# Performance work log

Hardware: AMD Instinct MI355X
Metric: run time of the kernel (lower is better)

Reference implementation:

```python
import jax, jax.numpy as jnp
import numpy as np

NPML = 50
B, NZ, NX = 4, 1024, 1024


def diff_using_roll(x, dim, forward=True):
    # First-order staggered-grid difference via circular roll (PML absorbs the
    # wrap-around, matching seistorch's roll-based stencil).
    if forward:
        return jnp.roll(x, -1, axis=dim) - x
    return x - jnp.roll(x, 1, axis=dim)


def _pml_profile(nz, nx, npml):
    # Quadratic damping profile, zero in interior, rising in the PML pad.
    iz = np.arange(nz, dtype=np.float32)
    ix = np.arange(nx, dtype=np.float32)
    dz = np.maximum(npml - iz, iz - (nz - 1 - npml))
    dx = np.maximum(npml - ix, ix - (nx - 1 - npml))
    dz = np.clip(dz, 0.0, None) / npml
    dx = np.clip(dx, 0.0, None) / npml
    prof = np.maximum(dz[:, None], dx[None, :]) ** 2
    return jnp.asarray(100.0 * prof, dtype=jnp.float32)


def setup_inputs() -> dict:
    key = jax.random.key(0)
    ks = jax.random.split(key, 8)
    vp = 3000.0 + 500.0 * jax.random.uniform(ks[0], (NZ, NX), dtype=jnp.float32)
    vs = 1700.0 + 300.0 * jax.random.uniform(ks[1], (NZ, NX), dtype=jnp.float32)
    rho = 2100.0 + 300.0 * jax.random.uniform(ks[2], (NZ, NX), dtype=jnp.float32)
    vx = jax.random.normal(ks[3], (B, NZ, NX), dtype=jnp.float32)
    vz = jax.random.normal(ks[4], (B, NZ, NX), dtype=jnp.float32)
    txx = jax.random.normal(ks[5], (B, NZ, NX), dtype=jnp.float32)
    tzz = jax.random.normal(ks[6], (B, NZ, NX), dtype=jnp.float32)
    txz = jax.random.normal(ks[7], (B, NZ, NX), dtype=jnp.float32)
    dt = jnp.float32(0.001)
    h = jnp.float32(10.0)     # 10 m grid spacing
    d = _pml_profile(NZ, NX, NPML)
    return {"vp": vp, "vs": vs, "rho": rho, "vx": vx, "vz": vz,
            "txx": txx, "tzz": tzz, "txz": txz, "dt": dt, "h": h, "d": d}


def reference(vp, vs, rho, vx, vz, txx, tzz, txz, dt, h, d):
    # Elastic wave equation time step with PML damping (seistorch _time_step).
    lame_lambda = rho * (vp * vp - 2.0 * vs * vs)  # [NZ,NX], broadcasts over shots
    lame_mu = rho * vs * vs

    vx_x = diff_using_roll(vx, 2, False)
    vz_z = diff_using_roll(vz, 1, True)
    vx_z = diff_using_roll(vx, 1, True)
    vz_x = diff_using_roll(vz, 2, True)

    c = 0.5 * dt * d
    inv = 1.0 / (1.0 + c)
    dth = dt / h

    y_txx = inv * (dth * ((lame_lambda + 2.0 * lame_mu) * vx_x + lame_lambda * vz_z) + (1.0 - c) * txx)
    y_tzz = inv * (dth * ((lame_lambda + 2.0 * lame_mu) * vz_z + lame_lambda * vx_x) + (1.0 - c) * tzz)
    y_txz = inv * (dt * lame_mu / h * (vz_x + vx_z) + (1.0 - c) * txz)

    txx_x = diff_using_roll(y_txx, 2, True)
    txz_z = diff_using_roll(y_txz, 1, False)
    tzz_z = diff_using_roll(y_tzz, 1, False)
    txz_x = diff_using_roll(y_txz, 2, False)

    y_vx = inv * (dth / rho * (txx_x + txz_z) + (1.0 - c) * vx)
    y_vz = inv * (dth / rho * (txz_x + tzz_z) + (1.0 - c) * vz)

    return (y_vx, y_vz, y_txx, y_tzz, y_txz)
```

## Files before the change

kernel.cpp:

```cpp
#include <hip/hip_runtime.h>


constexpr int Bn = 4, NZ = 1024, NX = 1024;
constexpr int PLANE = NZ * NX;
constexpr int NPTS = Bn * PLANE;
constexpr int R = 8;
constexpr int NSTRIP = NZ / R;
constexpr int LOG_NSTRIP = 7;

__global__ __launch_bounds__(256, 2) void fused_wave_kernel(
    const float* __restrict__ vp, const float* __restrict__ vs,
    const float* __restrict__ rho, const float* __restrict__ vx,
    const float* __restrict__ vz, const float* __restrict__ txx,
    const float* __restrict__ tzz, const float* __restrict__ txz,
    const float* __restrict__ dtp, const float* __restrict__ hp,
    const float* __restrict__ dpml,
    float* __restrict__ y_vx, float* __restrict__ y_vz,
    float* __restrict__ y_txx, float* __restrict__ y_tzz,
    float* __restrict__ y_txz)
{
    __shared__ float s_txx[3][NX];
    __shared__ float s_tzz[3][NX];
    __shared__ float s_txz[3][NX];

    const int tid = threadIdx.x;
    const int x0 = tid * 4;
    const int xm1 = (x0 - 1) & (NX - 1);
    const int xp4 = (x0 + 4) & (NX - 1);
    const int strip = blockIdx.x & (NSTRIP - 1);
    const int b = blockIdx.x >> LOG_NSTRIP;
    const int z0 = strip * R;
    const size_t fb = (size_t)b * PLANE;

    const float dt = dtp[0], h = hp[0];
    const float dth = dt / h;

    const int r0 = (z0 - 1) & (NZ - 1);
    const int r1 = z0;
    const size_t rb0 = fb + (size_t)r0 * NX;
    const size_t rb1 = fb + (size_t)r1 * NX;
    const int m0 = r0 * NX;

    float4 cvx = *(const float4*)(vx + rb0 + x0);
    float4 cvz = *(const float4*)(vz + rb0 + x0);
    float4 nvx = *(const float4*)(vx + rb1 + x0);
    float4 nvz = *(const float4*)(vz + rb1 + x0);
    float  cvxm = vx[rb0 + xm1];
    float  cvzp = vz[rb0 + xp4];
    float4 ctxx = *(const float4*)(txx + rb0 + x0);
    float4 ctzz = *(const float4*)(tzz + rb0 + x0);
    float4 ctxz = *(const float4*)(txz + rb0 + x0);
    float4 cvp = *(const float4*)(vp + m0 + x0);
    float4 cvs = *(const float4*)(vs + m0 + x0);
    float4 crh = *(const float4*)(rho + m0 + x0);
    float4 cd  = *(const float4*)(dpml + m0 + x0);

#pragma unroll
    for (int k = 0; k <= R; ++k) {
        const int r = (z0 - 1 + k) & (NZ - 1);
        const size_t rowb = fb + (size_t)r * NX;

        float4 n2vx, n2vz, ntxx, ntzz, ntxz, nvp, nvs, nrh, nd;
        float  nvxm = 0.f, nvzp = 0.f;
        if (k < R) {
            const int rn  = (z0 + k) & (NZ - 1);
            const int rn2 = (z0 + k + 1) & (NZ - 1);
            const size_t rbn  = fb + (size_t)rn * NX;
            const size_t rbn2 = fb + (size_t)rn2 * NX;
            const int mn = rn * NX;
            n2vx = *(const float4*)(vx + rbn2 + x0);
            n2vz = *(const float4*)(vz + rbn2 + x0);
            nvxm = vx[rbn + xm1];
            nvzp = vz[rbn + xp4];
            ntxx = *(const float4*)(txx + rbn + x0);
            ntzz = *(const float4*)(tzz + rbn + x0);
            ntxz = *(const float4*)(txz + rbn + x0);
            nvp = *(const float4*)(vp + mn + x0);
            nvs = *(const float4*)(vs + mn + x0);
            nrh = *(const float4*)(rho + mn + x0);
            nd  = *(const float4*)(dpml + mn + x0);
        }

        float fvx[5]  = {cvxm, cvx.x, cvx.y, cvx.z, cvx.w};
        float fvz[5]  = {cvz.x, cvz.y, cvz.z, cvz.w, cvzp};
        float fvx1[4] = {nvx.x, nvx.y, nvx.z, nvx.w};
        float fvz1[4] = {nvz.x, nvz.y, nvz.z, nvz.w};
        float ftxxo[4] = {ctxx.x, ctxx.y, ctxx.z, ctxx.w};
        float ftzzo[4] = {ctzz.x, ctzz.y, ctzz.z, ctzz.w};
        float ftxzo[4] = {ctxz.x, ctxz.y, ctxz.z, ctxz.w};
        float fvp[4] = {cvp.x, cvp.y, cvp.z, cvp.w};
        float fvs[4] = {cvs.x, cvs.y, cvs.z, cvs.w};
        float frh[4] = {crh.x, crh.y, crh.z, crh.w};
        float fd[4]  = {cd.x, cd.y, cd.z, cd.w};

        float o_txx[4], o_tzz[4], o_txz[4], inv[4], omc[4];
#pragma unroll
        for (int i = 0; i < 4; ++i) {
            float lam = frh[i] * (fvp[i] * fvp[i] - 2.0f * fvs[i] * fvs[i]);
            float mu  = frh[i] * fvs[i] * fvs[i];
            float vx_x = fvx[i + 1] - fvx[i];
            float vz_z = fvz1[i] - fvz[i];
            float vx_z = fvx1[i] - fvx[i + 1];
            float vz_x = fvz[i + 1] - fvz[i];
            float c = 0.5f * dt * fd[i];
            inv[i] = 1.0f / (1.0f + c);
            omc[i] = 1.0f - c;
            float lp2m = lam + 2.0f * mu;
            o_txx[i] = inv[i] * (dth * (lp2m * vx_x + lam * vz_z) + omc[i] * ftxxo[i]);
            o_tzz[i] = inv[i] * (dth * (lp2m * vz_z + lam * vx_x) + omc[i] * ftzzo[i]);
            o_txz[i] = inv[i] * (dth * mu * (vz_x + vx_z) + omc[i] * ftxzo[i]);
        }

        const int slot = k % 3;
        const int pslot = (k + 2) % 3;
        *(float4*)&s_txx[slot][x0] = make_float4(o_txx[0], o_txx[1], o_txx[2], o_txx[3]);
        *(float4*)&s_tzz[slot][x0] = make_float4(o_tzz[0], o_tzz[1], o_tzz[2], o_tzz[3]);
        *(float4*)&s_txz[slot][x0] = make_float4(o_txz[0], o_txz[1], o_txz[2], o_txz[3]);
        if (k > 0) {
            *(float4*)(y_txx + rowb + x0) = make_float4(o_txx[0], o_txx[1], o_txx[2], o_txx[3]);
            *(float4*)(y_tzz + rowb + x0) = make_float4(o_tzz[0], o_tzz[1], o_tzz[2], o_tzz[3]);
            *(float4*)(y_txz + rowb + x0) = make_float4(o_txz[0], o_txz[1], o_txz[2], o_txz[3]);
        }

        asm volatile("s_waitcnt lgkmcnt(0)" ::: "memory");
        __builtin_amdgcn_s_barrier();

        if (k > 0) {
            float  txxp4v = s_txx[slot][xp4];
            float  txzm1v = s_txz[slot][xm1];
            float4 txzzm = *(const float4*)&s_txz[pslot][x0];
            float4 tzzzm = *(const float4*)&s_tzz[pslot][x0];

            float ftxx5[5] = {o_txx[0], o_txx[1], o_txx[2], o_txx[3], txxp4v};
            float ftxz5[5] = {txzm1v, o_txz[0], o_txz[1], o_txz[2], o_txz[3]};
            float ftxzzm[4] = {txzzm.x, txzzm.y, txzzm.z, txzzm.w};
            float ftzzzm[4] = {tzzzm.x, tzzzm.y, tzzzm.z, tzzzm.w};
            float fvxc[4] = {cvx.x, cvx.y, cvx.z, cvx.w};
            float fvzc[4] = {cvz.x, cvz.y, cvz.z, cvz.w};

            float o_vx[4], o_vz[4];
#pragma unroll
            for (int i = 0; i < 4; ++i) {
                float txx_x = ftxx5[i + 1] - ftxx5[i];
                float txz_z = ftxz5[i + 1] - ftxzzm[i];
                float tzz_z = o_tzz[i] - ftzzzm[i];
                float txz_x = ftxz5[i + 1] - ftxz5[i];
                float s = dth / frh[i];
                o_vx[i] = inv[i] * (s * (txx_x + txz_z) + omc[i] * fvxc[i]);
                o_vz[i] = inv[i] * (s * (txz_x + tzz_z) + omc[i] * fvzc[i]);
            }
            *(float4*)(y_vx + rowb + x0) = make_float4(o_vx[0], o_vx[1], o_vx[2], o_vx[3]);
            *(float4*)(y_vz + rowb + x0) = make_float4(o_vz[0], o_vz[1], o_vz[2], o_vz[3]);
        }

        cvx = nvx; cvz = nvz;
        nvx = n2vx; nvz = n2vz;
        cvxm = nvxm; cvzp = nvzp;
        ctxx = ntxx; ctzz = ntzz; ctxz = ntxz;
        cvp = nvp; cvs = nvs; crh = nrh; cd = nd;
    }
}

extern "C" void kernel_launch(void* const* d_in, const int* in_sizes, int n_in,
                              void* d_out, int out_size, void* d_ws, size_t ws_size,
                              hipStream_t stream) {
    const float* vp  = (const float*)d_in[0];
    const float* vs  = (const float*)d_in[1];
    const float* rho = (const float*)d_in[2];
    const float* vx  = (const float*)d_in[3];
    const float* vz  = (const float*)d_in[4];
    const float* txx = (const float*)d_in[5];
    const float* tzz = (const float*)d_in[6];
    const float* txz = (const float*)d_in[7];
    const float* dtp = (const float*)d_in[8];
    const float* hp  = (const float*)d_in[9];
    const float* dpm = (const float*)d_in[10];

    float* out   = (float*)d_out;
    float* y_vx  = out;
    float* y_vz  = out + (size_t)NPTS;
    float* y_txx = out + 2 * (size_t)NPTS;
    float* y_tzz = out + 3 * (size_t)NPTS;
    float* y_txz = out + 4 * (size_t)NPTS;

    dim3 block(256);
    dim3 grid(Bn * NSTRIP);
    fused_wave_kernel<<<grid, block, 0, stream>>>(vp, vs, rho, vx, vz, txx, tzz, txz,
                                                  dtp, hp, dpm,
                                                  y_vx, y_vz, y_txx, y_tzz, y_txz);
}
```

Measured before the change: 37.18 us.

## Replace shared-memory halo exchange with wave shuffles and register-carried rows

Removes the LDS stress buffers and the per-row block barrier. Horizontal neighbours of the stress field are now exchanged with wave-level shuffles. At wave boundaries, lanes 0 and 63 redundantly recompute the neighbouring txx/txz value from extra scalar global loads. The previous row's tzz/txz values are carried in registers instead of LDS. This also drops the one-row-ahead register prefetch: each iteration now loads its own rows, which may expose more load latency. The occupancy hint in launch bounds is relaxed.

```diff
diff --git a/kernel.cpp b/kernel.cpp
--- a/kernel.cpp
+++ b/kernel.cpp
@@ -8,7 +8,7 @@
 constexpr int NSTRIP = NZ / R;
 constexpr int LOG_NSTRIP = 7;
 
-__global__ __launch_bounds__(256, 2) void fused_wave_kernel(
+__global__ __launch_bounds__(256) void fused_wave_kernel(
     const float* __restrict__ vp, const float* __restrict__ vs,
     const float* __restrict__ rho, const float* __restrict__ vx,
     const float* __restrict__ vz, const float* __restrict__ txx,
@@ -19,11 +19,8 @@
     float* __restrict__ y_txx, float* __restrict__ y_tzz,
     float* __restrict__ y_txz)
 {
-    __shared__ float s_txx[3][NX];
-    __shared__ float s_tzz[3][NX];
-    __shared__ float s_txz[3][NX];
-
     const int tid = threadIdx.x;
+    const int lane = tid & 63;
     const int x0 = tid * 4;
     const int xm1 = (x0 - 1) & (NX - 1);
     const int xp4 = (x0 + 4) & (NX - 1);
@@ -36,49 +33,52 @@
     const float dth = dt / h;
 
     const int r0 = (z0 - 1) & (NZ - 1);
-    const int r1 = z0;
     const size_t rb0 = fb + (size_t)r0 * NX;
-    const size_t rb1 = fb + (size_t)r1 * NX;
-    const int m0 = r0 * NX;
-
     float4 cvx = *(const float4*)(vx + rb0 + x0);
     float4 cvz = *(const float4*)(vz + rb0 + x0);
-    float4 nvx = *(const float4*)(vx + rb1 + x0);
-    float4 nvz = *(const float4*)(vz + rb1 + x0);
     float  cvxm = vx[rb0 + xm1];
     float  cvzp = vz[rb0 + xp4];
-    float4 ctxx = *(const float4*)(txx + rb0 + x0);
-    float4 ctzz = *(const float4*)(tzz + rb0 + x0);
-    float4 ctxz = *(const float4*)(txz + rb0 + x0);
-    float4 cvp = *(const float4*)(vp + m0 + x0);
-    float4 cvs = *(const float4*)(vs + m0 + x0);
-    float4 crh = *(const float4*)(rho + m0 + x0);
-    float4 cd  = *(const float4*)(dpml + m0 + x0);
+    float  cvxp = 0.f, cvzm = 0.f;
+    if (lane == 63) cvxp = vx[rb0 + xp4];
+    if (lane == 0)  cvzm = vz[rb0 + xm1];
+
+    float p_tzz[4] = {0, 0, 0, 0};
+    float p_txz[4] = {0, 0, 0, 0};
 
 #pragma unroll
     for (int k = 0; k <= R; ++k) {
-        const int r = (z0 - 1 + k) & (NZ - 1);
-        const size_t rowb = fb + (size_t)r * NX;
+        const int r  = (z0 - 1 + k) & (NZ - 1);
+        const int rp = (r + 1) & (NZ - 1);
+        const size_t rowb  = fb + (size_t)r * NX;
+        const size_t rowbp = fb + (size_t)rp * NX;
+        const int mrow = r * NX;
 
-        float4 n2vx, n2vz, ntxx, ntzz, ntxz, nvp, nvs, nrh, nd;
-        float  nvxm = 0.f, nvzp = 0.f;
-        if (k < R) {
-            const int rn  = (z0 + k) & (NZ - 1);
-            const int rn2 = (z0 + k + 1) & (NZ - 1);
-            const size_t rbn  = fb + (size_t)rn * NX;
-            const size_t rbn2 = fb + (size_t)rn2 * NX;
-            const int mn = rn * NX;
-            n2vx = *(const float4*)(vx + rbn2 + x0);
-            n2vz = *(const float4*)(vz + rbn2 + x0);
-            nvxm = vx[rbn + xm1];
-            nvzp = vz[rbn + xp4];
-            ntxx = *(const float4*)(txx + rbn + x0);
-            ntzz = *(const float4*)(tzz + rbn + x0);
-            ntxz = *(const float4*)(txz + rbn + x0);
-            nvp = *(const float4*)(vp + mn + x0);
-            nvs = *(const float4*)(vs + mn + x0);
-            nrh = *(const float4*)(rho + mn + x0);
-            nd  = *(const float4*)(dpml + mn + x0);
+        float4 nvx = *(const float4*)(vx + rowbp + x0);
+        float4 nvz = *(const float4*)(vz + rowbp + x0);
+        float  nvxm = vx[rowbp + xm1];
+        float  nvzp = vz[rowbp + xp4];
+        float  nvxp = 0.f, nvzm = 0.f;
+        float4 ctxx = *(const float4*)(txx + rowb + x0);
+        float4 ctzz = *(const float4*)(tzz + rowb + x0);
+        float4 ctxz = *(const float4*)(txz + rowb + x0);
+        float4 cvp = *(const float4*)(vp + mrow + x0);
+        float4 cvs = *(const float4*)(vs + mrow + x0);
+        float4 crh = *(const float4*)(rho + mrow + x0);
+        float4 cd  = *(const float4*)(dpml + mrow + x0);
+
+        float txxh_o = 0.f, vph = 0.f, vsh = 0.f, rhh = 0.f, dh = 0.f;
+        float txzh_o = 0.f, vsl = 0.f, rhl = 0.f, dl = 0.f;
+        if (lane == 63) {
+            nvxp   = vx[rowbp + xp4];
+            txxh_o = txx[rowb + xp4];
+            vph = vp[mrow + xp4]; vsh = vs[mrow + xp4];
+            rhh = rho[mrow + xp4]; dh = dpml[mrow + xp4];
+        }
+        if (lane == 0) {
+            nvzm   = vz[rowbp + xm1];
+            txzh_o = txz[rowb + xm1];
+            vsl = vs[mrow + xm1]; rhl = rho[mrow + xm1];
+            dl = dpml[mrow + xm1];
         }
 
         float fvx[5]  = {cvxm, cvx.x, cvx.y, cvx.z, cvx.w};
@@ -111,30 +111,38 @@
             o_txz[i] = inv[i] * (dth * mu * (vz_x + vx_z) + omc[i] * ftxzo[i]);
         }
 
-        const int slot = k % 3;
-        const int pslot = (k + 2) % 3;
-        *(float4*)&s_txx[slot][x0] = make_float4(o_txx[0], o_txx[1], o_txx[2], o_txx[3]);
-        *(float4*)&s_tzz[slot][x0] = make_float4(o_tzz[0], o_tzz[1], o_tzz[2], o_tzz[3]);
-        *(float4*)&s_txz[slot][x0] = make_float4(o_txz[0], o_txz[1], o_txz[2], o_txz[3]);
+        float txxh, txzh;
+        {
+            float lamh = rhh * (vph * vph - 2.0f * vsh * vsh);
+            float muh  = rhh * vsh * vsh;
+            float vxxh = cvxp - cvx.w;
+            float vzzh = nvzp - cvzp;
+            float ch = 0.5f * dt * dh;
+            txxh = (1.0f / (1.0f + ch)) *
+                   (dth * ((lamh + 2.0f * muh) * vxxh + lamh * vzzh) +
+                    (1.0f - ch) * txxh_o);
+        }
+        {
+            float mul = rhl * vsl * vsl;
+            float vzxl = cvz.x - cvzm;
+            float vxzl = nvxm - cvxm;
+            float cl = 0.5f * dt * dl;
+            txzh = (1.0f / (1.0f + cl)) *
+                   (dth * mul * (vzxl + vxzl) + (1.0f - cl) * txzh_o);
+        }
+
+        float txxp4 = __shfl_down(o_txx[0], 1);
+        float txzm1 = __shfl_up(o_txz[3], 1);
+        if (lane == 63) txxp4 = txxh;
+        if (lane == 0)  txzm1 = txzh;
+
         if (k > 0) {
             *(float4*)(y_txx + rowb + x0) = make_float4(o_txx[0], o_txx[1], o_txx[2], o_txx[3]);
             *(float4*)(y_tzz + rowb + x0) = make_float4(o_tzz[0], o_tzz[1], o_tzz[2], o_tzz[3]);
             *(float4*)(y_txz + rowb + x0) = make_float4(o_txz[0], o_txz[1], o_txz[2], o_txz[3]);
-        }
 
-        asm volatile("s_waitcnt lgkmcnt(0)" ::: "memory");
-        __builtin_amdgcn_s_barrier();
-
-        if (k > 0) {
-            float  txxp4v = s_txx[slot][xp4];
-            float  txzm1v = s_txz[slot][xm1];
-            float4 txzzm = *(const float4*)&s_txz[pslot][x0];
-            float4 tzzzm = *(const float4*)&s_tzz[pslot][x0];
-
-            float ftxx5[5] = {o_txx[0], o_txx[1], o_txx[2], o_txx[3], txxp4v};
-            float ftxz5[5] = {txzm1v, o_txz[0], o_txz[1], o_txz[2], o_txz[3]};
-            float ftxzzm[4] = {txzzm.x, txzzm.y, txzzm.z, txzzm.w};
-            float ftzzzm[4] = {tzzzm.x, tzzzm.y, tzzzm.z, tzzzm.w};
+            float ftxx5[5] = {o_txx[0], o_txx[1], o_txx[2], o_txx[3], txxp4};
+            float ftxz5[5] = {txzm1, o_txz[0], o_txz[1], o_txz[2], o_txz[3]};
             float fvxc[4] = {cvx.x, cvx.y, cvx.z, cvx.w};
             float fvzc[4] = {cvz.x, cvz.y, cvz.z, cvz.w};
 
@@ -142,8 +150,8 @@
 #pragma unroll
             for (int i = 0; i < 4; ++i) {
                 float txx_x = ftxx5[i + 1] - ftxx5[i];
-                float txz_z = ftxz5[i + 1] - ftxzzm[i];
-                float tzz_z = o_tzz[i] - ftzzzm[i];
+                float txz_z = ftxz5[i + 1] - p_txz[i];
+                float tzz_z = o_tzz[i] - p_tzz[i];
                 float txz_x = ftxz5[i + 1] - ftxz5[i];
                 float s = dth / frh[i];
                 o_vx[i] = inv[i] * (s * (txx_x + txz_z) + omc[i] * fvxc[i]);
@@ -154,10 +162,10 @@
         }
 
         cvx = nvx; cvz = nvz;
-        nvx = n2vx; nvz = n2vz;
         cvxm = nvxm; cvzp = nvzp;
-        ctxx = ntxx; ctzz = ntzz; ctxz = ntxz;
-        cvp = nvp; cvs = nvs; crh = nrh; cd = nd;
+        cvxp = nvxp; cvzm = nvzm;
+#pragma unroll
+        for (int i = 0; i < 4; ++i) { p_tzz[i] = o_tzz[i]; p_txz[i] = o_txz[i]; }
     }
 }
 
```

Result: no change. 37.28 us (+0.3%).
